# Optimization experiments

Hardware: AMD Instinct MI355X
Metric: run time of the kernel (lower is better)

The kernel has to match this reference:

```python
import jax, jax.numpy as jnp
import numpy as np


def _lc2d(x, W, b, kh, kw):
    """Locally connected conv: distinct (Cout,Cin,kh,kw) kernel per output location.
    x: [B,Cin,H,W]; W: [Hout,Wout,Cout,Cin,kh,kw]; b: [Hout,Wout,Cout].
    Kernel size == stride, so each output pixel sees a disjoint kh x kw patch."""
    B, C, H, Wd = x.shape
    Hout, Wout = H // kh, Wd // kw
    patches = x.reshape(B, C, Hout, kh, Wout, kw)  # [b,c,i,k,j,l]
    out = jnp.einsum('bcikjl,ijockl->boij', patches, W)
    return out + b.transpose(2, 0, 1)[None]  # [B,Cout,Hout,Wout]


def setup_inputs() -> dict:
    key = jax.random.key(0)
    ks = jax.random.split(key, 11)

    def u(k, shape, fan_in):
        bound = 1.0 / np.sqrt(fan_in)
        return jax.random.uniform(k, shape, jnp.float32, -bound, bound)

    B = 4096
    x = jax.random.normal(ks[0], (B, 6, 60, 60), jnp.float32)
    info = jax.random.normal(ks[1], (B, 2), jnp.float32)
    # b0: 20x20 locations, Conv2d(6->32, 3x3)
    W0 = u(ks[2], (20, 20, 32, 6, 3, 3), 6 * 9)
    B0 = u(ks[3], (20, 20, 32), 6 * 9)
    # b1: 10x10 locations, Conv2d(32->64, 2x2)
    W1 = u(ks[4], (10, 10, 64, 32, 2, 2), 32 * 4)
    B1 = u(ks[5], (10, 10, 64), 32 * 4)
    # b2: 2x2 locations, Conv2d(64->128, 5x5)
    W2 = u(ks[6], (2, 2, 128, 64, 5, 5), 64 * 25)
    B2 = u(ks[7], (2, 2, 128), 64 * 25)
    # classifier Linear(514, 2); stored as [in, out]
    Wc = u(ks[8], (514, 2), 514)
    bc = u(ks[9], (2,), 514)
    return {"x": x, "info": info, "W0": W0, "B0": B0, "W1": W1, "B1": B1,
            "W2": W2, "B2": B2, "Wc": Wc, "bc": bc}


def reference(x, info, W0, B0, W1, B1, W2, B2, Wc, bc):
    h = jnp.tanh(_lc2d(x, W0, B0, 3, 3))   # [B,32,20,20]
    h = jnp.tanh(_lc2d(h, W1, B1, 2, 2))   # [B,64,10,10]
    h = jnp.tanh(_lc2d(h, W2, B2, 5, 5))   # [B,128,2,2]
    h = h.reshape(h.shape[0], -1)          # [B,512]
    h = jnp.concatenate([h, info], axis=1)  # [B,514]
    logits = h @ Wc + bc                    # [B,2]
    return jax.nn.softmax(logits, axis=1)
```

## Files before the change

kernel.cpp:

```cpp
#include <hip/hip_runtime.h>

typedef short short8 __attribute__((ext_vector_type(8)));
typedef float floatx4 __attribute__((ext_vector_type(4)));

__device__ __forceinline__ float bf2f(unsigned short u) {
  union { unsigned int i; float f; } v; v.i = ((unsigned int)u) << 16; return v.f;
}
__device__ __forceinline__ unsigned short f2bf(float f) {
  union { float f; unsigned int i; } v; v.f = f;
  return (unsigned short)((v.i + 0x7fffu + ((v.i >> 16) & 1u)) >> 16);
}
__device__ __forceinline__ float ftanh(float x) {
  float e = __expf(2.f * x);
  return 1.f - 2.f / (e + 1.f);
}

__global__ __launch_bounds__(256) void k_permute(const float* __restrict__ W0,
                                                 const float* __restrict__ W1,
                                                 const float* __restrict__ W2,
                                                 unsigned short* __restrict__ W0f,
                                                 unsigned short* __restrict__ W1f,
                                                 unsigned short* __restrict__ W2f) {
  int idx = blockIdx.x * 256 + threadIdx.x;
  int sec = idx / 819200;
  int q = idx - sec * 819200;
  int frag = q >> 9, li = q & 511;
  int lane = li >> 3, e = li & 7;
  int n = lane & 15, quad = lane >> 4;
  if (sec == 0) {
    int loc = frag >> 2, nt = (frag >> 1) & 1, ks = frag & 1;
    int kk = (ks << 5) + (quad << 3) + e;
    int co = (nt << 4) + n;
    unsigned short v = 0;
    if (kk < 54) {
      int l = kk / 18, cr = kk - l * 18;
      v = f2bf(W0[loc * 1728 + co * 54 + cr * 3 + l]);
    }
    W0f[q] = v;
  } else if (sec == 1) {
    int loc = frag >> 4, nt = (frag >> 2) & 3, ks = frag & 3;
    int kk = (ks << 5) + (quad << 3) + e;
    int kl = kk >> 5, c = kk & 31, co = (nt << 4) + n;
    W1f[q] = f2bf(W1[(size_t)loc * 8192 + (co << 7) + (c << 2) + kl]);
  } else {
    int g = frag / 50, ks = frag - g * 50;
    int loc = g >> 3, nt = g & 7;
    int kk = (ks << 5) + (quad << 3) + e;
    int kl5 = kk >> 6, c = kk & 63, co = (nt << 4) + n;
    W2f[q] = f2bf(W2[(size_t)loc * 204800 + co * 1600 + c * 25 + kl5]);
  }
}

__global__ __launch_bounds__(256, 4) void k_l0(const float* __restrict__ x,
                                               const short8* __restrict__ W0f,
                                               const float* __restrict__ B0,
                                               unsigned short* __restrict__ h0) {
  const int t = threadIdx.x;
  const int b0 = blockIdx.x << 4;
  const int i = blockIdx.y;
  __shared__ __align__(16) unsigned short sX[16 * 1128];

  for (int e = t; e < 4320; e += 256) {
    int b = e / 270, rem = e - b * 270;
    int cr = rem / 15, q = rem - cr * 15;
    float4 xv = *(const float4*)&x[(size_t)(b0 + b) * 21600 + (cr / 3) * 3600 +
                                   (3 * i + (cr % 3)) * 60 + (q << 2)];
    float vals[4] = {xv.x, xv.y, xv.z, xv.w};
#pragma unroll
    for (int m = 0; m < 4; ++m) {
      int col = (q << 2) + m;
      int j = col / 3, l = col - j * 3;
      sX[b * 1128 + j * 56 + l * 18 + cr] = f2bf(vals[m]);
    }
  }
  for (int e = t; e < 320; e += 256) {
    int b = e / 20, j = e - b * 20;
    *(unsigned int*)&sX[b * 1128 + j * 56 + 54] = 0u;
  }
  __syncthreads();

  const int lane = t & 63, w = t >> 6;
  const int n16 = lane & 15, quad = lane >> 4;
  const floatx4 z = {0.f, 0.f, 0.f, 0.f};

  for (int jj = 0; jj < 5; ++jj) {
    const int j = w * 5 + jj;
    const int loc = i * 20 + j;
    short8 a0 = *(const short8*)&sX[n16 * 1128 + j * 56 + (quad << 3)];
    short8 a1 = {};
    if (quad < 3) a1 = *(const short8*)&sX[n16 * 1128 + j * 56 + 32 + (quad << 3)];

    short8 b00 = W0f[(((loc << 1) + 0) << 1) * 64 + 0 * 64 + lane];
    short8 b01 = W0f[((((loc << 1) + 0) << 1) + 1) * 64 + lane];
    short8 b10 = W0f[((((loc << 1) + 1) << 1) + 0) * 64 + lane];
    short8 b11 = W0f[((((loc << 1) + 1) << 1) + 1) * 64 + lane];

    floatx4 acc0 = z, acc1 = z;
    acc0 = __builtin_amdgcn_mfma_f32_16x16x32_bf16(a0, b00, acc0, 0, 0, 0);
    acc0 = __builtin_amdgcn_mfma_f32_16x16x32_bf16(a1, b01, acc0, 0, 0, 0);
    acc1 = __builtin_amdgcn_mfma_f32_16x16x32_bf16(a0, b10, acc1, 0, 0, 0);
    acc1 = __builtin_amdgcn_mfma_f32_16x16x32_bf16(a1, b11, acc1, 0, 0, 0);

    const int o_off = (((i >> 1) * 10 + (j >> 1)) << 7) + (((i & 1) * 2 + (j & 1)) << 5);
    float bias0 = B0[loc * 32 + n16];
    float bias1 = B0[loc * 32 + 16 + n16];
#pragma unroll
    for (int reg = 0; reg < 4; ++reg) {
      int bb = b0 + (quad << 2) + reg;
      h0[(size_t)bb * 12800 + o_off + n16]      = f2bf(ftanh(acc0[reg] + bias0));
      h0[(size_t)bb * 12800 + o_off + 16 + n16] = f2bf(ftanh(acc1[reg] + bias1));
    }
  }
}

__global__ __launch_bounds__(256, 6) void k_l1(const unsigned short* __restrict__ h0,
                                               const short8* __restrict__ W1f,
                                               const float* __restrict__ B1,
                                               unsigned short* __restrict__ h1) {
  const int t = threadIdx.x, lane = t & 63, w = t >> 6;
  const int loc = blockIdx.y;
  const int i = loc / 10, j = loc - i * 10;
  const int b0 = (blockIdx.x << 6) + (w << 4);
  const int n16 = lane & 15, quad = lane >> 4;

  short8 a[4];
#pragma unroll
  for (int ks = 0; ks < 4; ++ks)
    a[ks] = *(const short8*)&h0[(size_t)(b0 + n16) * 12800 + (loc << 7) + (ks << 5) + (quad << 3)];

  const floatx4 z = {0.f, 0.f, 0.f, 0.f};
  floatx4 acc[4] = {z, z, z, z};
#pragma unroll
  for (int ks = 0; ks < 4; ++ks)
#pragma unroll
    for (int nt = 0; nt < 4; ++nt)
      acc[nt] = __builtin_amdgcn_mfma_f32_16x16x32_bf16(
          a[ks], W1f[(((loc << 2) + nt) << 2) * 64 + ks * 64 + lane], acc[nt], 0, 0, 0);

  const int loc2 = (i / 5) * 2 + (j / 5);
  const int kl5 = (i % 5) * 5 + (j % 5);
  const int obase = loc2 * 1600 + (kl5 << 6);
#pragma unroll
  for (int nt = 0; nt < 4; ++nt) {
    int co = (nt << 4) + n16;
    float bias = B1[(loc << 6) + co];
#pragma unroll
    for (int reg = 0; reg < 4; ++reg) {
      int bb = b0 + (quad << 2) + reg;
      h1[(size_t)bb * 6400 + obase + co] = f2bf(ftanh(acc[nt][reg] + bias));
    }
  }
}

__global__ __launch_bounds__(256, 4) void k_l2(const unsigned short* __restrict__ h1,
                                               const short8* __restrict__ W2f,
                                               const float* __restrict__ B2,
                                               float* __restrict__ h2) {
  const int t = threadIdx.x, lane = t & 63, w = t >> 6;
  const int nh = blockIdx.y;
  const int loc = blockIdx.z;
  const int b0 = (blockIdx.x << 6) + (w << 4);
  const int n16 = lane & 15, quad = lane >> 4;

  const floatx4 z = {0.f, 0.f, 0.f, 0.f};
  floatx4 acc[4] = {z, z, z, z};
  const unsigned short* arow = h1 + (size_t)(b0 + n16) * 6400 + loc * 1600 + (quad << 3);
  const short8* wbase = W2f + (size_t)(((loc << 3) + (nh << 2)) * 50) * 64 + lane;

  for (int ks = 0; ks < 50; ++ks) {
    short8 a = *(const short8*)&arow[ks << 5];
#pragma unroll
    for (int nt4 = 0; nt4 < 4; ++nt4)
      acc[nt4] = __builtin_amdgcn_mfma_f32_16x16x32_bf16(
          a, wbase[(nt4 * 50 + ks) * 64], acc[nt4], 0, 0, 0);
  }

#pragma unroll
  for (int nt4 = 0; nt4 < 4; ++nt4) {
    int co = (((nh << 2) + nt4) << 4) + n16;
    float bias = B2[(loc << 7) + co];
#pragma unroll
    for (int reg = 0; reg < 4; ++reg) {
      int bb = b0 + (quad << 2) + reg;
      h2[(size_t)bb * 512 + (co << 2) + loc] = ftanh(acc[nt4][reg] + bias);
    }
  }
}

__global__ __launch_bounds__(256) void k_cls(const float* __restrict__ h2,
                                             const float* __restrict__ info,
                                             const float* __restrict__ Wc,
                                             const float* __restrict__ bc,
                                             float* __restrict__ out) {
  const int l = threadIdx.x & 63;
  const int b = blockIdx.x * 4 + (threadIdx.x >> 6);
  const float* hrow = h2 + (size_t)b * 512;
  float p0 = 0.f, p1 = 0.f;
#pragma unroll
  for (int f = 0; f < 512; f += 64) {
    float h = hrow[f + l];
    p0 = fmaf(h, Wc[2 * (f + l)], p0);
    p1 = fmaf(h, Wc[2 * (f + l) + 1], p1);
  }
#pragma unroll
  for (int m = 32; m; m >>= 1) {
    p0 += __shfl_xor(p0, m, 64);
    p1 += __shfl_xor(p1, m, 64);
  }
  if (l == 0) {
    float i0 = info[2 * b], i1 = info[2 * b + 1];
    float l0 = p0 + i0 * Wc[1024] + i1 * Wc[1026] + bc[0];
    float l1 = p1 + i0 * Wc[1025] + i1 * Wc[1027] + bc[1];
    float mx = fmaxf(l0, l1);
    float e0 = __expf(l0 - mx), e1 = __expf(l1 - mx);
    float inv = 1.f / (e0 + e1);
    out[2 * b]     = e0 * inv;
    out[2 * b + 1] = e1 * inv;
  }
}

extern "C" void kernel_launch(void* const* d_in, const int* in_sizes, int n_in,
                              void* d_out, int out_size, void* d_ws, size_t ws_size,
                              hipStream_t stream) {
  const float* x    = (const float*)d_in[0];
  const float* info = (const float*)d_in[1];
  const float* W0   = (const float*)d_in[2];
  const float* B0   = (const float*)d_in[3];
  const float* W1   = (const float*)d_in[4];
  const float* B1   = (const float*)d_in[5];
  const float* W2   = (const float*)d_in[6];
  const float* B2   = (const float*)d_in[7];
  const float* Wc   = (const float*)d_in[8];
  const float* bc   = (const float*)d_in[9];
  float* out = (float*)d_out;

  char* ws = (char*)d_ws;
  unsigned short* h0  = (unsigned short*)ws;
  unsigned short* h1  = (unsigned short*)(ws + 104857600);
  float*          h2  = (float*)(ws + 157286400);
  unsigned short* W0f = (unsigned short*)(ws + 165675008);
  unsigned short* W1f = (unsigned short*)(ws + 167313408);
  unsigned short* W2f = (unsigned short*)(ws + 168951808);

  k_permute<<<dim3(9600),     dim3(256), 0, stream>>>(W0, W1, W2, W0f, W1f, W2f);
  k_l0     <<<dim3(256, 20),  dim3(256), 0, stream>>>(x, (const short8*)W0f, B0, h0);
  k_l1     <<<dim3(64, 100),  dim3(256), 0, stream>>>(h0, (const short8*)W1f, B1, h1);
  k_l2     <<<dim3(64, 2, 4), dim3(256), 0, stream>>>(h1, (const short8*)W2f, B2, h2);
  k_cls    <<<dim3(1024),     dim3(256), 0, stream>>>(h2, info, Wc, bc, out);
}
```

Measured before the change: 648.5 us.

## Fuse layer1 and layer2 via shared memory; rework layer0 staging to per-thread patches

Layer 1 and layer 2 now run in one kernel. Each block computes the 25 layer-1 locations feeding one layer-2 location for 16 batch rows and keeps the bf16 activations in LDS, so the h1 round trip through global memory goes away. Layer 0 now uses 320 threads, one per (batch, output column), each gathering its own 3x3x6 patch. This changes the K ordering of the packed W0 to match the raw weight layout and drops the old transpose scatter. Risks: the fused kernel has a small grid (1024 blocks) and a large LDS footprint at 2 blocks per CU, and the layer-0 loads are now scalar and strided.

After: 603.3 us. 7.0% less time.

```diff
diff --git a/kernel.cpp b/kernel.cpp
--- a/kernel.cpp
+++ b/kernel.cpp
@@ -3,9 +3,6 @@
 typedef short short8 __attribute__((ext_vector_type(8)));
 typedef float floatx4 __attribute__((ext_vector_type(4)));
 
-__device__ __forceinline__ float bf2f(unsigned short u) {
-  union { unsigned int i; float f; } v; v.i = ((unsigned int)u) << 16; return v.f;
-}
 __device__ __forceinline__ unsigned short f2bf(float f) {
   union { float f; unsigned int i; } v; v.f = f;
   return (unsigned short)((v.i + 0x7fffu + ((v.i >> 16) & 1u)) >> 16);
@@ -32,10 +29,7 @@
     int kk = (ks << 5) + (quad << 3) + e;
     int co = (nt << 4) + n;
     unsigned short v = 0;
-    if (kk < 54) {
-      int l = kk / 18, cr = kk - l * 18;
-      v = f2bf(W0[loc * 1728 + co * 54 + cr * 3 + l]);
-    }
+    if (kk < 54) v = f2bf(W0[loc * 1728 + co * 54 + kk]);
     W0f[q] = v;
   } else if (sec == 1) {
     int loc = frag >> 4, nt = (frag >> 2) & 3, ks = frag & 3;
@@ -51,7 +45,7 @@
   }
 }
 
-__global__ __launch_bounds__(256, 4) void k_l0(const float* __restrict__ x,
+__global__ __launch_bounds__(320, 5) void k_l0(const float* __restrict__ x,
                                                const short8* __restrict__ W0f,
                                                const float* __restrict__ B0,
                                                unsigned short* __restrict__ h0) {
@@ -60,22 +54,27 @@
   const int i = blockIdx.y;
   __shared__ __align__(16) unsigned short sX[16 * 1128];
 
-  for (int e = t; e < 4320; e += 256) {
-    int b = e / 270, rem = e - b * 270;
-    int cr = rem / 15, q = rem - cr * 15;
-    float4 xv = *(const float4*)&x[(size_t)(b0 + b) * 21600 + (cr / 3) * 3600 +
-                                   (3 * i + (cr % 3)) * 60 + (q << 2)];
-    float vals[4] = {xv.x, xv.y, xv.z, xv.w};
-#pragma unroll
-    for (int m = 0; m < 4; ++m) {
-      int col = (q << 2) + m;
-      int j = col / 3, l = col - j * 3;
-      sX[b * 1128 + j * 56 + l * 18 + cr] = f2bf(vals[m]);
-    }
-  }
-  for (int e = t; e < 320; e += 256) {
-    int b = e / 20, j = e - b * 20;
-    *(unsigned int*)&sX[b * 1128 + j * 56 + 54] = 0u;
+  {
+    const int b = t / 20, j = t - (t / 20) * 20;
+    const float* xb = x + (size_t)(b0 + b) * 21600 + (3 * i) * 60 + 3 * j;
+    unsigned short* dst = &sX[b * 1128 + j * 56];
+    int c = 0, r = 0;
+#pragma unroll
+    for (int p = 0; p < 9; ++p) {
+      const float* pa = xb + c * 3600 + r * 60;
+      float a0 = pa[0], a1 = pa[1], a2 = pa[2];
+      ++r; if (r == 3) { r = 0; ++c; }
+      const float* pb = xb + c * 3600 + r * 60;
+      float b0v = pb[0], b1v = pb[1], b2v = pb[2];
+      ++r; if (r == 3) { r = 0; ++c; }
+      unsigned int w0 = (unsigned int)f2bf(a0) | ((unsigned int)f2bf(a1) << 16);
+      unsigned int w1 = (unsigned int)f2bf(a2) | ((unsigned int)f2bf(b0v) << 16);
+      unsigned int w2 = (unsigned int)f2bf(b1v) | ((unsigned int)f2bf(b2v) << 16);
+      *(unsigned int*)&dst[p * 6]     = w0;
+      *(unsigned int*)&dst[p * 6 + 2] = w1;
+      *(unsigned int*)&dst[p * 6 + 4] = w2;
+    }
+    *(unsigned int*)&dst[54] = 0u;
   }
   __syncthreads();
 
@@ -83,17 +82,18 @@
   const int n16 = lane & 15, quad = lane >> 4;
   const floatx4 z = {0.f, 0.f, 0.f, 0.f};
 
-  for (int jj = 0; jj < 5; ++jj) {
-    const int j = w * 5 + jj;
+#pragma unroll
+  for (int jj = 0; jj < 4; ++jj) {
+    const int j = (w << 2) + jj;
     const int loc = i * 20 + j;
     short8 a0 = *(const short8*)&sX[n16 * 1128 + j * 56 + (quad << 3)];
     short8 a1 = {};
     if (quad < 3) a1 = *(const short8*)&sX[n16 * 1128 + j * 56 + 32 + (quad << 3)];
 
-    short8 b00 = W0f[(((loc << 1) + 0) << 1) * 64 + 0 * 64 + lane];
-    short8 b01 = W0f[((((loc << 1) + 0) << 1) + 1) * 64 + lane];
-    short8 b10 = W0f[((((loc << 1) + 1) << 1) + 0) * 64 + lane];
-    short8 b11 = W0f[((((loc << 1) + 1) << 1) + 1) * 64 + lane];
+    short8 b00 = W0f[((loc << 2) + 0) * 64 + lane];
+    short8 b01 = W0f[((loc << 2) + 1) * 64 + lane];
+    short8 b10 = W0f[((loc << 2) + 2) * 64 + lane];
+    short8 b11 = W0f[((loc << 2) + 3) * 64 + lane];
 
     floatx4 acc0 = z, acc1 = z;
     acc0 = __builtin_amdgcn_mfma_f32_16x16x32_bf16(a0, b00, acc0, 0, 0, 0);
@@ -113,76 +113,68 @@
   }
 }
 
-__global__ __launch_bounds__(256, 6) void k_l1(const unsigned short* __restrict__ h0,
-                                               const short8* __restrict__ W1f,
-                                               const float* __restrict__ B1,
-                                               unsigned short* __restrict__ h1) {
+__global__ __launch_bounds__(256, 2) void k_l12(const unsigned short* __restrict__ h0,
+                                                const short8* __restrict__ W1f,
+                                                const float* __restrict__ B1,
+                                                const short8* __restrict__ W2f,
+                                                const float* __restrict__ B2,
+                                                float* __restrict__ h2) {
   const int t = threadIdx.x, lane = t & 63, w = t >> 6;
-  const int loc = blockIdx.y;
-  const int i = loc / 10, j = loc - i * 10;
-  const int b0 = (blockIdx.x << 6) + (w << 4);
   const int n16 = lane & 15, quad = lane >> 4;
-
-  short8 a[4];
-#pragma unroll
-  for (int ks = 0; ks < 4; ++ks)
-    a[ks] = *(const short8*)&h0[(size_t)(b0 + n16) * 12800 + (loc << 7) + (ks << 5) + (quad << 3)];
+  const int b0 = blockIdx.x << 4;
+  const int q = blockIdx.y;
+  const int i0 = (q >> 1) * 5, j0 = (q & 1) * 5;
+
+  __shared__ __align__(16) unsigned short sH[16 * 1608];
 
   const floatx4 z = {0.f, 0.f, 0.f, 0.f};
-  floatx4 acc[4] = {z, z, z, z};
-#pragma unroll
-  for (int ks = 0; ks < 4; ++ks)
-#pragma unroll
-    for (int nt = 0; nt < 4; ++nt)
-      acc[nt] = __builtin_amdgcn_mfma_f32_16x16x32_bf16(
-          a[ks], W1f[(((loc << 2) + nt) << 2) * 64 + ks * 64 + lane], acc[nt], 0, 0, 0);
-
-  const int loc2 = (i / 5) * 2 + (j / 5);
-  const int kl5 = (i % 5) * 5 + (j % 5);
-  const int obase = loc2 * 1600 + (kl5 << 6);
-#pragma unroll
-  for (int nt = 0; nt < 4; ++nt) {
-    int co = (nt << 4) + n16;
-    float bias = B1[(loc << 6) + co];
+
+  for (int li = w; li < 25; li += 4) {
+    const int di = li / 5, dj = li - di * 5;
+    const int loc = (i0 + di) * 10 + (j0 + dj);
+
+    short8 a[4];
+#pragma unroll
+    for (int ks = 0; ks < 4; ++ks)
+      a[ks] = *(const short8*)&h0[(size_t)(b0 + n16) * 12800 + (loc << 7) + (ks << 5) + (quad << 3)];
+
+    floatx4 acc[4] = {z, z, z, z};
+#pragma unroll
+    for (int ks = 0; ks < 4; ++ks)
+#pragma unroll
+      for (int nt = 0; nt < 4; ++nt)
+        acc[nt] = __builtin_amdgcn_mfma_f32_16x16x32_bf16(
+            a[ks], W1f[(((loc << 2) + nt) << 2) * 64 + ks * 64 + lane], acc[nt], 0, 0, 0);
+
+#pragma unroll
+    for (int nt = 0; nt < 4; ++nt) {
+      float bias = B1[(loc << 6) + (nt << 4) + n16];
+      int col = (li << 6) + (nt << 4) + n16;
+#pragma unroll
+      for (int reg = 0; reg < 4; ++reg)
+        sH[((quad << 2) + reg) * 1608 + col] = f2bf(ftanh(acc[nt][reg] + bias));
+    }
+  }
+  __syncthreads();
+
+  floatx4 acc0 = z, acc1 = z;
+  const short8* wb0 = W2f + (size_t)(((q << 3) + (w << 1)) * 50) * 64 + lane;
+  const short8* wb1 = wb0 + (size_t)50 * 64;
+  for (int ks = 0; ks < 50; ++ks) {
+    short8 a = *(const short8*)&sH[n16 * 1608 + (ks << 5) + (quad << 3)];
+    acc0 = __builtin_amdgcn_mfma_f32_16x16x32_bf16(a, wb0[ks * 64], acc0, 0, 0, 0);
+    acc1 = __builtin_amdgcn_mfma_f32_16x16x32_bf16(a, wb1[ks * 64], acc1, 0, 0, 0);
+  }
+
+#pragma unroll
+  for (int u = 0; u < 2; ++u) {
+    const floatx4& ac = u ? acc1 : acc0;
+    int co = (((w << 1) + u) << 4) + n16;
+    float bias = B2[(q << 7) + co];
 #pragma unroll
     for (int reg = 0; reg < 4; ++reg) {
       int bb = b0 + (quad << 2) + reg;
-      h1[(size_t)bb * 6400 + obase + co] = f2bf(ftanh(acc[nt][reg] + bias));
-    }
-  }
-}
-
-__global__ __launch_bounds__(256, 4) void k_l2(const unsigned short* __restrict__ h1,
-                                               const short8* __restrict__ W2f,
-                                               const float* __restrict__ B2,
-                                               float* __restrict__ h2) {
-  const int t = threadIdx.x, lane = t & 63, w = t >> 6;
-  const int nh = blockIdx.y;
-  const int loc = blockIdx.z;
-  const int b0 = (blockIdx.x << 6) + (w << 4);
-  const int n16 = lane & 15, quad = lane >> 4;
-
-  const floatx4 z = {0.f, 0.f, 0.f, 0.f};
-  floatx4 acc[4] = {z, z, z, z};
-  const unsigned short* arow = h1 + (size_t)(b0 + n16) * 6400 + loc * 1600 + (quad << 3);
-  const short8* wbase = W2f + (size_t)(((loc << 3) + (nh << 2)) * 50) * 64 + lane;
-
-  for (int ks = 0; ks < 50; ++ks) {
-    short8 a = *(const short8*)&arow[ks << 5];
-#pragma unroll
-    for (int nt4 = 0; nt4 < 4; ++nt4)
-      acc[nt4] = __builtin_amdgcn_mfma_f32_16x16x32_bf16(
-          a, wbase[(nt4 * 50 + ks) * 64], acc[nt4], 0, 0, 0);
-  }
-
-#pragma unroll
-  for (int nt4 = 0; nt4 < 4; ++nt4) {
-    int co = (((nh << 2) + nt4) << 4) + n16;
-    float bias = B2[(loc << 7) + co];
-#pragma unroll
-    for (int reg = 0; reg < 4; ++reg) {
-      int bb = b0 + (quad << 2) + reg;
-      h2[(size_t)bb * 512 + (co << 2) + loc] = ftanh(acc[nt4][reg] + bias);
+      h2[(size_t)bb * 512 + (co << 2) + q] = ftanh(ac[reg] + bias);
     }
   }
 }
@@ -236,15 +228,14 @@
 
   char* ws = (char*)d_ws;
   unsigned short* h0  = (unsigned short*)ws;
-  unsigned short* h1  = (unsigned short*)(ws + 104857600);
-  float*          h2  = (float*)(ws + 157286400);
-  unsigned short* W0f = (unsigned short*)(ws + 165675008);
-  unsigned short* W1f = (unsigned short*)(ws + 167313408);
-  unsigned short* W2f = (unsigned short*)(ws + 168951808);
-
-  k_permute<<<dim3(9600),     dim3(256), 0, stream>>>(W0, W1, W2, W0f, W1f, W2f);
-  k_l0     <<<dim3(256, 20),  dim3(256), 0, stream>>>(x, (const short8*)W0f, B0, h0);
-  k_l1     <<<dim3(64, 100),  dim3(256), 0, stream>>>(h0, (const short8*)W1f, B1, h1);
-  k_l2     <<<dim3(64, 2, 4), dim3(256), 0, stream>>>(h1, (const short8*)W2f, B2, h2);
-  k_cls    <<<dim3(1024),     dim3(256), 0, stream>>>(h2, info, Wc, bc, out);
-}
+  float*          h2  = (float*)(ws + 104857600);
+  unsigned short* W0f = (unsigned short*)(ws + 113246208);
+  unsigned short* W1f = (unsigned short*)(ws + 114884608);
+  unsigned short* W2f = (unsigned short*)(ws + 116523008);
+
+  k_permute<<<dim3(9600),    dim3(256), 0, stream>>>(W0, W1, W2, W0f, W1f, W2f);
+  k_l0     <<<dim3(256, 20), dim3(320), 0, stream>>>(x, (const short8*)W0f, B0, h0);
+  k_l12    <<<dim3(256, 4),  dim3(256), 0, stream>>>(h0, (const short8*)W1f, B1,
+                                                     (const short8*)W2f, B2, h2);
+  k_cls    <<<dim3(1024),    dim3(256), 0, stream>>>(h2, info, Wc, bc, out);
+}
```
